# Kernel tuning notes

Hardware: AMD Instinct MI355X
Metric: run time of the kernel (lower is better)

## Reference

```python
import jax, jax.numpy as jnp
import numpy as np


def setup_inputs() -> dict:
    key = jax.random.key(0)
    k1, k2, k3, k4 = jax.random.split(key, 4)
    B, T, C, H = 8, 2048, 1024, 128
    x = jax.random.normal(k1, (B, T, C), dtype=jnp.float32)
    Wq = jax.random.normal(k2, (C, H), dtype=jnp.float32) * (C ** -0.5)
    Wk = jax.random.normal(k3, (C, H), dtype=jnp.float32) * (C ** -0.5)
    Wv = jax.random.normal(k4, (C, H), dtype=jnp.float32) * (C ** -0.5)
    return {
        "x": x, "Wq": Wq, "Wk": Wk, "Wv": Wv,
        "gamma_fast_logit": jnp.float32(0.0),
        "gamma_medium_logit": jnp.float32(2.0),
        "gamma_slow_logit": jnp.float32(4.0),
        "alpha_logits": jnp.zeros((3,), dtype=jnp.float32),
    }


def _temporal_bias(T, gamma_fast_logit, gamma_medium_logit, gamma_slow_logit, alpha_logits):
    # delta_t[i,j] = max(i-j, 0)
    i = jnp.arange(T)[:, None]
    j = jnp.arange(T)[None, :]
    delta_t = jnp.maximum(i - j, 0).astype(jnp.float32)  # (T, T)
    gf = jax.nn.sigmoid(gamma_fast_logit) * 0.3 + 0.6
    gm = jax.nn.sigmoid(gamma_medium_logit) * 0.15 + 0.85
    gs = jax.nn.sigmoid(gamma_slow_logit) * 0.05 + 0.95
    alpha = jax.nn.softmax(alpha_logits)
    mix = (alpha[0] * jnp.power(gf, delta_t)
           + alpha[1] * jnp.power(gm, delta_t)
           + alpha[2] * jnp.power(gs, delta_t))
    return jnp.log(mix + 1e-8)  # (T, T)


def reference(x, Wq, Wk, Wv, gamma_fast_logit, gamma_medium_logit, gamma_slow_logit, alpha_logits):
    B, T, C = x.shape
    H = Wq.shape[1]
    q = x @ Wq  # (B, T, H)
    k = x @ Wk
    v = x @ Wv
    scale = H ** -0.5
    wei = jnp.einsum('bth,bsh->bts', q, k) * scale  # (B, T, T)
    bias = _temporal_bias(T, gamma_fast_logit, gamma_medium_logit, gamma_slow_logit, alpha_logits)
    wei = wei + bias[None, :, :]
    causal = jnp.tril(jnp.ones((T, T), dtype=bool))
    wei = jnp.where(causal[None, :, :], wei, -jnp.inf)
    wei = jax.nn.softmax(wei, axis=-1)
    out = jnp.einsum('bts,bsh->bth', wei, v)  # (B, T, H)
    return out
```

## Files before the change

kernel.cpp:

```cpp
#include <hip/hip_runtime.h>
#include <hip/hip_bf16.h>
#include <cstdint>

typedef __attribute__((ext_vector_type(8))) short bf16x8;
typedef __attribute__((ext_vector_type(4))) float f32x4;

#define T_SEQ 2048
#define NB    8
#define CDIM  1024
#define HDIM  128
#define NQB   32

__device__ __forceinline__ float exp2fast(float x) { return __builtin_amdgcn_exp2f(x); }
__device__ __forceinline__ float log2fast(float x) { return __builtin_amdgcn_logf(x); }

__device__ __forceinline__ short f2bf(float f) {
  unsigned u = __float_as_uint(f);
  u += 0x7fff + ((u >> 16) & 1);
  return (short)(u >> 16);
}

__device__ __forceinline__ float bf2f(short s) {
  return __uint_as_float(((unsigned)(unsigned short)s) << 16);
}

__device__ __forceinline__ unsigned pk2(float a, float b) {
  return (unsigned)(unsigned short)f2bf(a) | ((unsigned)(unsigned short)f2bf(b) << 16);
}

__device__ __forceinline__ void gload_lds16(const void* gsrc, void* lds_base_uniform) {
  __builtin_amdgcn_global_load_lds(
      (const __attribute__((address_space(1))) unsigned int*)gsrc,
      (__attribute__((address_space(3))) unsigned int*)lds_base_uniform,
      16, 0, 0);
}

__global__ void msta_bias_kernel(const float* gfl, const float* gml, const float* gsl,
                                 const float* al, float* tab) {
  int d = blockIdx.x * 256 + threadIdx.x;
  if (d >= T_SEQ) return;
  float gf = 0.30f / (1.f + __expf(-gfl[0])) + 0.60f;
  float gm = 0.15f / (1.f + __expf(-gml[0])) + 0.85f;
  float gs = 0.05f / (1.f + __expf(-gsl[0])) + 0.95f;
  float a0 = al[0], a1 = al[1], a2 = al[2];
  float mx = fmaxf(a0, fmaxf(a1, a2));
  float e0 = __expf(a0 - mx), e1 = __expf(a1 - mx), e2 = __expf(a2 - mx);
  float inv = 1.f / (e0 + e1 + e2);
  float fd = (float)d;
  float mix = e0 * inv * exp2fast(fd * log2fast(gf))
            + e1 * inv * exp2fast(fd * log2fast(gm))
            + e2 * inv * exp2fast(fd * log2fast(gs));
  tab[d] = log2fast(mix + 1e-8f);
}

__global__ void msta_wt_kernel(const float* Wq, const float* Wk, const float* Wv, short* wt) {
  int idx = blockIdx.x * 256 + threadIdx.x;
  int m = idx >> 17;
  int r = idx & 131071;
  int n = r >> 10;
  int kv = r & 1023;
  const float* W = (m == 0) ? Wq : ((m == 1) ? Wk : Wv);
  float v = W[kv * HDIM + n];
  if (m == 0) v *= 0.08838834764831845f * 1.4426950408889634f;
  int c  = m * 128 + n;
  int t  = kv >> 6, kk = (kv >> 5) & 1, hi = (kv >> 3) & 3, e = kv & 7;
  int cf = c >> 4,  lo = c & 15;
  int si = (((t * 2 + kk) * 24 + cf) * 64 + (hi * 16 + lo)) * 8 + e;
  wt[si] = f2bf(v);
}

__global__ __launch_bounds__(256) void msta_qkv_kernel(
    const float* __restrict__ x, const short* __restrict__ wt,
    short* __restrict__ q, short* __restrict__ k, short* __restrict__ vt) {
  __shared__ short lds[32 * 384];

  const int tid  = threadIdx.x;
  const int lane = tid & 63;
  const int w    = tid >> 6;
  const int lo   = lane & 15, hi = lane >> 4;
  const int bid  = blockIdx.x;
  const int xcd  = bid & 7;
  const int j    = bid >> 3;
  const int r0   = (xcd * 64 + j) * 32;

  const int xrow = tid >> 3, xc8 = tid & 7;
  const float* xsrc = x + (size_t)(r0 + xrow) * CDIM + xc8 * 8;
  const int xdst = xrow * 128 + ((xc8 * 16) ^ ((xrow & 7) << 4));

  f32x4 acc[2][6];
  #pragma unroll
  for (int f = 0; f < 2; f++)
    #pragma unroll
    for (int jf = 0; jf < 6; jf++)
      acc[f][jf] = (f32x4){0.f, 0.f, 0.f, 0.f};

  float4 xa, xb;
  auto xload = [&](int t) {
    const float* s = xsrc + t * 64;
    xa = *(const float4*)s;
    xb = *(const float4*)(s + 4);
  };
  auto xwrite = [&]() {
    uint4 u;
    u.x = pk2(xa.x, xa.y); u.y = pk2(xa.z, xa.w);
    u.z = pk2(xb.x, xb.y); u.w = pk2(xb.z, xb.w);
    *(uint4*)((char*)lds + xdst) = u;
  };

  xload(0);
  for (int t = 0; t < 16; ++t) {
    xwrite();
    __syncthreads();
    if (t < 15) xload(t + 1);

    bf16x8 Bv[2][6];
    #pragma unroll
    for (int kk = 0; kk < 2; kk++)
      #pragma unroll
      for (int jf = 0; jf < 6; jf++) {
        int si = (((t * 2 + kk) * 24 + (w * 6 + jf)) * 64 + lane) * 8;
        Bv[kk][jf] = *(const bf16x8*)(wt + si);
      }

    #pragma unroll
    for (int kk = 0; kk < 2; kk++) {
      bf16x8 A[2];
      #pragma unroll
      for (int f = 0; f < 2; f++) {
        int r = f * 16 + lo;
        A[f] = *(const bf16x8*)((const char*)lds + r * 128 +
                                ((kk * 64 + hi * 16) ^ ((r & 7) << 4)));
      }
      #pragma unroll
      for (int jf = 0; jf < 6; jf++) {
        acc[0][jf] = __builtin_amdgcn_mfma_f32_16x16x32_bf16(A[0], Bv[kk][jf], acc[0][jf], 0, 0, 0);
        acc[1][jf] = __builtin_amdgcn_mfma_f32_16x16x32_bf16(A[1], Bv[kk][jf], acc[1][jf], 0, 0, 0);
      }
    }
    __syncthreads();
  }

  #pragma unroll
  for (int f = 0; f < 2; f++) {
    #pragma unroll
    for (int jf = 0; jf < 6; jf++) {
      int c = w * 96 + jf * 16 + lo;
      int row0 = f * 16 + hi * 4;
      f32x4 a = acc[f][jf];
      #pragma unroll
      for (int rg = 0; rg < 4; rg++)
        lds[(row0 + rg) * 384 + c] = f2bf(a[rg]);
    }
  }
  __syncthreads();

  #pragma unroll
  for (int p = 0; p < 2; p++) {
    int g = tid + p * 256;
    int row = g >> 4, c16 = g & 15;
    *(bf16x8*)(q + (size_t)(r0 + row) * HDIM + c16 * 8) =
        *(const bf16x8*)(lds + row * 384 + c16 * 8);
    *(bf16x8*)(k + (size_t)(r0 + row) * HDIM + c16 * 8) =
        *(const bf16x8*)(lds + row * 384 + 128 + c16 * 8);
  }
  const int bb = r0 >> 11, tt0 = r0 & 2047;
  #pragma unroll
  for (int p = 0; p < 2; p++) {
    int g = tid + p * 256;
    int h = g >> 2, rowg = g & 3;
    bf16x8 vv;
    #pragma unroll
    for (int i = 0; i < 8; i++)
      vv[i] = lds[(rowg * 8 + i) * 384 + 256 + h];
    *(bf16x8*)(vt + ((size_t)bb * HDIM + h) * T_SEQ + tt0 + rowg * 8) = vv;
  }
}

template <int SP>
__global__ __launch_bounds__(256) void msta_attn_kernel(
    const short* __restrict__ q, const short* __restrict__ kg,
    const short* __restrict__ vt, const float* __restrict__ bias_tab,
    float* __restrict__ out, short* __restrict__ opart, float2* __restrict__ ml) {
  __shared__ short Ks[64 * 128];
  __shared__ short Vs[128 * 64];
  __shared__ short Ps[4][16 * 64];

  const int tid  = threadIdx.x;
  const int lane = tid & 63;
  const int w    = tid >> 6;
  const int lo   = lane & 15, hi = lane >> 4;

  const int idx = blockIdx.x;
  const int b   = idx & 7;
  const int r_  = idx >> 3;
  const int qb  = (NQB - 1) - r_ / SP;
  const int sp  = r_ % SP;
  const int q0  = qb * 64;

  const int nt  = qb + 1;
  const int csz = (nt + SP - 1) / SP;
  const int t0  = sp * csz;
  const int t1  = (t0 + csz < nt) ? (t0 + csz) : nt;

  if (t0 >= t1) {
    if (SP > 1 && lane < 16) {
      int t = q0 + w * 16 + lane;
      ml[((size_t)sp * NB + b) * T_SEQ + t] = make_float2(-1e30f, 0.f);
    }
    return;
  }

  const short* kb = kg + (size_t)b * T_SEQ * HDIM;
  const short* vb = vt + (size_t)b * HDIM * T_SEQ;

  bf16x8 qf[4];
  const short* qbase = q + ((size_t)b * T_SEQ + q0 + w * 16 + lo) * HDIM;
  #pragma unroll
  for (int ks = 0; ks < 4; ks++)
    qf[ks] = *(const bf16x8*)(qbase + ks * 32 + hi * 8);

  const int s0i = (t1 - 1) * 64;
  const char* ksrc[4];
  const char* vsrc[4];
  #pragma unroll
  for (int i = 0; i < 4; i++) {
    int G = (w * 4 + i) * 64 + lane;
    { int r = G >> 4, g = G & 15;
      int c = (g & 8) | ((g & 7) ^ (r & 7));
      ksrc[i] = (const char*)(kb + (size_t)(s0i + r) * HDIM) + c * 16; }
    { int r = G >> 3, g = G & 7;
      int c = g ^ (r & 7);
      vsrc[i] = (const char*)(vb + (size_t)r * T_SEQ + s0i) + c * 16; }
  }
  auto stage = [&]() {
    #pragma unroll
    for (int i = 0; i < 4; i++) {
      gload_lds16(ksrc[i], (char*)Ks + (w * 4 + i) * 1024);
      ksrc[i] -= 64 * HDIM * 2;
      gload_lds16(vsrc[i], (char*)Vs + (w * 4 + i) * 1024);
      vsrc[i] -= 128;
    }
  };

  f32x4 oacc[8];
  #pragma unroll
  for (int jo = 0; jo < 8; jo++) oacc[jo] = (f32x4){0.f, 0.f, 0.f, 0.f};
  float mrow[4], lrow[4];
  #pragma unroll
  for (int rg = 0; rg < 4; rg++) { mrow[rg] = -1e30f; lrow[rg] = 0.f; }

  stage();
  __syncthreads();

  for (int t = t1 - 1; t >= t0; --t) {
    const int s0 = t * 64;

    f32x4 sacc[4];
    #pragma unroll
    for (int jf = 0; jf < 4; jf++) sacc[jf] = (f32x4){0.f, 0.f, 0.f, 0.f};
    __builtin_amdgcn_s_setprio(1);
    #pragma unroll
    for (int ks = 0; ks < 4; ks++) {
      #pragma unroll
      for (int jf = 0; jf < 4; jf++) {
        int s = jf * 16 + lo;
        int byteoff = s * 256 + ((ks * 64 + hi * 16) ^ ((s & 7) << 4));
        bf16x8 kf = *(const bf16x8*)((const char*)Ks + byteoff);
        sacc[jf] = __builtin_amdgcn_mfma_f32_16x16x32_bf16(qf[ks], kf, sacc[jf], 0, 0, 0);
      }
    }
    __builtin_amdgcn_s_setprio(0);

    float sv[4][4];
    #pragma unroll
    for (int jf = 0; jf < 4; jf++) {
      #pragma unroll
      for (int rg = 0; rg < 4; rg++) {
        int i_ = q0 + w * 16 + hi * 4 + rg;
        int j_ = s0 + jf * 16 + lo;
        int d = i_ - j_;
        sv[jf][rg] = (d >= 0) ? (sacc[jf][rg] + bias_tab[d]) : -1e30f;
      }
    }

    float mx[4];
    bool need = false;
    #pragma unroll
    for (int rg = 0; rg < 4; rg++) {
      float v = fmaxf(fmaxf(sv[0][rg], sv[1][rg]), fmaxf(sv[2][rg], sv[3][rg]));
      v = fmaxf(v, __shfl_xor(v, 1));
      v = fmaxf(v, __shfl_xor(v, 2));
      v = fmaxf(v, __shfl_xor(v, 4));
      v = fmaxf(v, __shfl_xor(v, 8));
      mx[rg] = v;
      need |= (v > mrow[rg]);
    }
    if (__any((int)need)) {
      #pragma unroll
      for (int rg = 0; rg < 4; rg++) {
        float mnew = fmaxf(mrow[rg], mx[rg]);
        float sc = exp2fast(mrow[rg] - mnew);
        mrow[rg] = mnew;
        lrow[rg] *= sc;
        #pragma unroll
        for (int jo = 0; jo < 8; jo++) oacc[jo][rg] *= sc;
      }
    }

    float psum[4] = {0.f, 0.f, 0.f, 0.f};
    #pragma unroll
    for (int jf = 0; jf < 4; jf++) {
      #pragma unroll
      for (int rg = 0; rg < 4; rg++) {
        float p = exp2fast(sv[jf][rg] - mrow[rg]);
        psum[rg] += p;
        int prow = hi * 4 + rg;
        int pcol = jf * 16 + lo;
        int byteoff = prow * 128 + ((pcol * 2) ^ ((prow & 7) << 4));
        *(short*)((char*)Ps[w] + byteoff) = f2bf(p);
      }
    }
    #pragma unroll
    for (int rg = 0; rg < 4; rg++) {
      float s = psum[rg];
      s += __shfl_xor(s, 1); s += __shfl_xor(s, 2);
      s += __shfl_xor(s, 4); s += __shfl_xor(s, 8);
      lrow[rg] += s;
    }

    __builtin_amdgcn_s_setprio(1);
    #pragma unroll
    for (int ks = 0; ks < 2; ks++) {
      int pbyte = lo * 128 + ((ks * 64 + hi * 16) ^ ((lo & 7) << 4));
      bf16x8 pf = *(const bf16x8*)((const char*)Ps[w] + pbyte);
      #pragma unroll
      for (int jo = 0; jo < 8; jo++) {
        int h = jo * 16 + lo;
        int vbyte = h * 128 + ((ks * 64 + hi * 16) ^ ((h & 7) << 4));
        bf16x8 vf = *(const bf16x8*)((const char*)Vs + vbyte);
        oacc[jo] = __builtin_amdgcn_mfma_f32_16x16x32_bf16(pf, vf, oacc[jo], 0, 0, 0);
      }
    }
    __builtin_amdgcn_s_setprio(0);

    if (t > t0) {
      __syncthreads();
      stage();
      __syncthreads();
    }
  }

  if constexpr (SP == 1) {
    #pragma unroll
    for (int jo = 0; jo < 8; jo++) {
      #pragma unroll
      for (int rg = 0; rg < 4; rg++) {
        int t = q0 + w * 16 + hi * 4 + rg;
        out[((size_t)b * T_SEQ + t) * HDIM + jo * 16 + lo] = oacc[jo][rg] / lrow[rg];
      }
    }
  } else {
    #pragma unroll
    for (int jo = 0; jo < 8; jo++) {
      #pragma unroll
      for (int rg = 0; rg < 4; rg++) {
        int t = q0 + w * 16 + hi * 4 + rg;
        opart[(((size_t)sp * NB + b) * T_SEQ + t) * HDIM + jo * 16 + lo] = f2bf(oacc[jo][rg]);
      }
    }
    if (lo == 0) {
      #pragma unroll
      for (int rg = 0; rg < 4; rg++) {
        int t = q0 + w * 16 + hi * 4 + rg;
        ml[((size_t)sp * NB + b) * T_SEQ + t] = make_float2(mrow[rg], lrow[rg]);
      }
    }
  }
}

template <int SP>
__global__ __launch_bounds__(256) void msta_merge_kernel(
    const short* __restrict__ opart, const float2* __restrict__ ml,
    float* __restrict__ out) {
  int id  = blockIdx.x * 256 + threadIdx.x;
  int row = id >> 5;
  int c4  = id & 31;

  float2 v[SP];
  float m = -1e30f;
  #pragma unroll
  for (int sp = 0; sp < SP; sp++) {
    v[sp] = ml[(size_t)sp * (NB * T_SEQ) + row];
    if (v[sp].y > 0.f) m = fmaxf(m, v[sp].x);
  }
  float denom = 0.f;
  float wgt[SP];
  #pragma unroll
  for (int sp = 0; sp < SP; sp++) {
    wgt[sp] = (v[sp].y > 0.f) ? exp2fast(v[sp].x - m) : 0.f;
    denom += wgt[sp] * v[sp].y;
  }
  float4 acc = {0.f, 0.f, 0.f, 0.f};
  #pragma unroll
  for (int sp = 0; sp < SP; sp++) {
    if (wgt[sp] != 0.f) {
      ushort4 o = *(const ushort4*)(opart + ((size_t)sp * (NB * T_SEQ) + row) * HDIM + c4 * 4);
      acc.x += wgt[sp] * bf2f((short)o.x); acc.y += wgt[sp] * bf2f((short)o.y);
      acc.z += wgt[sp] * bf2f((short)o.z); acc.w += wgt[sp] * bf2f((short)o.w);
    }
  }
  float inv = 1.f / denom;
  float4 r = make_float4(acc.x * inv, acc.y * inv, acc.z * inv, acc.w * inv);
  *(float4*)(out + (size_t)row * HDIM + c4 * 4) = r;
}

extern "C" void kernel_launch(void* const* d_in, const int* in_sizes, int n_in,
                              void* d_out, int out_size, void* d_ws, size_t ws_size,
                              hipStream_t stream) {
  (void)in_sizes; (void)n_in; (void)out_size;
  const float* x   = (const float*)d_in[0];
  const float* Wq  = (const float*)d_in[1];
  const float* Wk  = (const float*)d_in[2];
  const float* Wv  = (const float*)d_in[3];
  const float* gfl = (const float*)d_in[4];
  const float* gml = (const float*)d_in[5];
  const float* gsl = (const float*)d_in[6];
  const float* al  = (const float*)d_in[7];
  float* out = (float*)d_out;

  char* wsb = (char*)d_ws;
  float*  bias_tab = (float*)wsb;
  short*  qw   = (short*)(wsb + 8192);
  short*  kw   = (short*)(wsb + 8192 + 1 * 4194304);
  short*  vtw  = (short*)(wsb + 8192 + 2 * 4194304);
  short*  wtw  = (short*)(wsb + 8192 + 3 * 4194304);
  short*  opart = (short*)(wsb + 14680064);

  const size_t need8 = 14680064 + 8ull * 4194304 + 8ull * 131072;
  const size_t need4 = 14680064 + 4ull * 4194304 + 4ull * 131072;

  msta_bias_kernel<<<8, 256, 0, stream>>>(gfl, gml, gsl, al, bias_tab);
  msta_wt_kernel<<<1536, 256, 0, stream>>>(Wq, Wk, Wv, wtw);
  msta_qkv_kernel<<<512, 256, 0, stream>>>(x, wtw, qw, kw, vtw);

  if (ws_size >= need8) {
    float2* mlp = (float2*)(wsb + 14680064 + 8ull * 4194304);
    msta_attn_kernel<8><<<NB * NQB * 8, 256, 0, stream>>>(qw, kw, vtw, bias_tab,
                                                          nullptr, opart, mlp);
    msta_merge_kernel<8><<<(NB * T_SEQ * 32) / 256, 256, 0, stream>>>(opart, mlp, out);
  } else if (ws_size >= need4) {
    float2* mlp = (float2*)(wsb + 14680064 + 4ull * 4194304);
    msta_attn_kernel<4><<<NB * NQB * 4, 256, 0, stream>>>(qw, kw, vtw, bias_tab,
                                                          nullptr, opart, mlp);
    msta_merge_kernel<4><<<(NB * T_SEQ * 32) / 256, 256, 0, stream>>>(opart, mlp, out);
  } else {
    msta_attn_kernel<1><<<NB * NQB, 256, 0, stream>>>(qw, kw, vtw, bias_tab,
                                                      out, nullptr, nullptr);
  }
}
```

Baseline: 92.53 us.

## Split QKV projection across two column halves and add separate relayout kernel

The QKV projection kernel now launches 1024 blocks, each computing half of the 384 output columns for a 32-row tile, instead of 512 blocks computing all columns. Accumulators are written in MFMA fragment order to a scratch buffer. A new relayout kernel then gathers them into row-major q/k and transposed v. The x loads also become nontemporal. This is meant to raise parallelism and lower register and LDS pressure, but it reads x twice and adds a kernel launch plus an extra scratch round trip with scalar gathered reads.

```diff
diff --git a/kernel.cpp b/kernel.cpp
--- a/kernel.cpp
+++ b/kernel.cpp
@@ -69,10 +69,10 @@
   wt[si] = f2bf(v);
 }
 
-__global__ __launch_bounds__(256) void msta_qkv_kernel(
+__global__ __launch_bounds__(256) void msta_qkv_gemm(
     const float* __restrict__ x, const short* __restrict__ wt,
-    short* __restrict__ q, short* __restrict__ k, short* __restrict__ vt) {
-  __shared__ short lds[32 * 384];
+    short* __restrict__ scratch) {
+  __shared__ short lds[32 * 64];
 
   const int tid  = threadIdx.x;
   const int lane = tid & 63;
@@ -81,24 +81,26 @@
   const int bid  = blockIdx.x;
   const int xcd  = bid & 7;
   const int j    = bid >> 3;
-  const int r0   = (xcd * 64 + j) * 32;
+  const int cid  = j & 1;
+  const int rowblk = j >> 1;
+  const int r0   = (xcd * 64 + rowblk) * 32;
 
   const int xrow = tid >> 3, xc8 = tid & 7;
   const float* xsrc = x + (size_t)(r0 + xrow) * CDIM + xc8 * 8;
   const int xdst = xrow * 128 + ((xc8 * 16) ^ ((xrow & 7) << 4));
 
-  f32x4 acc[2][6];
+  f32x4 acc[2][3];
   #pragma unroll
   for (int f = 0; f < 2; f++)
     #pragma unroll
-    for (int jf = 0; jf < 6; jf++)
+    for (int jf = 0; jf < 3; jf++)
       acc[f][jf] = (f32x4){0.f, 0.f, 0.f, 0.f};
 
-  float4 xa, xb;
+  f32x4 xa, xb;
   auto xload = [&](int t) {
-    const float* s = xsrc + t * 64;
-    xa = *(const float4*)s;
-    xb = *(const float4*)(s + 4);
+    const f32x4* s = (const f32x4*)(xsrc + t * 64);
+    xa = __builtin_nontemporal_load(s);
+    xb = __builtin_nontemporal_load(s + 1);
   };
   auto xwrite = [&]() {
     uint4 u;
@@ -113,12 +115,12 @@
     __syncthreads();
     if (t < 15) xload(t + 1);
 
-    bf16x8 Bv[2][6];
+    bf16x8 Bv[2][3];
     #pragma unroll
     for (int kk = 0; kk < 2; kk++)
       #pragma unroll
-      for (int jf = 0; jf < 6; jf++) {
-        int si = (((t * 2 + kk) * 24 + (w * 6 + jf)) * 64 + lane) * 8;
+      for (int jf = 0; jf < 3; jf++) {
+        int si = (((t * 2 + kk) * 24 + (cid * 12 + w * 3 + jf)) * 64 + lane) * 8;
         Bv[kk][jf] = *(const bf16x8*)(wt + si);
       }
 
@@ -132,7 +134,7 @@
                                 ((kk * 64 + hi * 16) ^ ((r & 7) << 4)));
       }
       #pragma unroll
-      for (int jf = 0; jf < 6; jf++) {
+      for (int jf = 0; jf < 3; jf++) {
         acc[0][jf] = __builtin_amdgcn_mfma_f32_16x16x32_bf16(A[0], Bv[kk][jf], acc[0][jf], 0, 0, 0);
         acc[1][jf] = __builtin_amdgcn_mfma_f32_16x16x32_bf16(A[1], Bv[kk][jf], acc[1][jf], 0, 0, 0);
       }
@@ -140,39 +142,66 @@
     __syncthreads();
   }
 
+  short* sb = scratch + (size_t)bid * 6144;
   #pragma unroll
   for (int f = 0; f < 2; f++) {
     #pragma unroll
-    for (int jf = 0; jf < 6; jf++) {
-      int c = w * 96 + jf * 16 + lo;
-      int row0 = f * 16 + hi * 4;
+    for (int jf = 0; jf < 3; jf++) {
       f32x4 a = acc[f][jf];
-      #pragma unroll
-      for (int rg = 0; rg < 4; rg++)
-        lds[(row0 + rg) * 384 + c] = f2bf(a[rg]);
-    }
-  }
-  __syncthreads();
-
-  #pragma unroll
-  for (int p = 0; p < 2; p++) {
-    int g = tid + p * 256;
-    int row = g >> 4, c16 = g & 15;
-    *(bf16x8*)(q + (size_t)(r0 + row) * HDIM + c16 * 8) =
-        *(const bf16x8*)(lds + row * 384 + c16 * 8);
-    *(bf16x8*)(k + (size_t)(r0 + row) * HDIM + c16 * 8) =
-        *(const bf16x8*)(lds + row * 384 + 128 + c16 * 8);
-  }
-  const int bb = r0 >> 11, tt0 = r0 & 2047;
-  #pragma unroll
-  for (int p = 0; p < 2; p++) {
-    int g = tid + p * 256;
-    int h = g >> 2, rowg = g & 3;
-    bf16x8 vv;
+      uint2 pr;
+      pr.x = pk2(a[0], a[1]);
+      pr.y = pk2(a[2], a[3]);
+      *(uint2*)(sb + (f * 3 + jf) * 1024 + tid * 4) = pr;
+    }
+  }
+}
+
+__device__ __forceinline__ short read_scr(const short* scratch, int rb, int row, int c) {
+  int xcd = rb >> 6, rowblk = rb & 63;
+  int cid = c / 192;
+  int cl  = c - cid * 192;
+  int w_  = cl / 48;
+  int jf  = (cl % 48) >> 4;
+  int lo_ = cl & 15;
+  int f_  = row >> 4;
+  int hi_ = (row >> 2) & 3;
+  int rg  = row & 3;
+  int bid = (((rowblk << 1) + cid) << 3) + xcd;
+  return scratch[(((size_t)bid * 6 + f_ * 3 + jf) << 10) + ((w_ * 64 + hi_ * 16 + lo_) << 2) + rg];
+}
+
+__global__ __launch_bounds__(256) void msta_relayout(
+    const short* __restrict__ scratch,
+    short* __restrict__ q, short* __restrict__ k, short* __restrict__ vt) {
+  const int tid = threadIdx.x;
+  if (blockIdx.x < 2048) {
+    int g   = blockIdx.x * 256 + tid;
+    int rb  = g >> 10;
+    int rem = g & 1023;
+    int row = rem >> 5;
+    int cg  = rem & 31;
+    int r0  = rb * 32;
+    bf16x8 v;
     #pragma unroll
     for (int i = 0; i < 8; i++)
-      vv[i] = lds[(rowg * 8 + i) * 384 + 256 + h];
-    *(bf16x8*)(vt + ((size_t)bb * HDIM + h) * T_SEQ + tt0 + rowg * 8) = vv;
+      v[i] = read_scr(scratch, rb, row, cg * 8 + i);
+    if (cg < 16)
+      *(bf16x8*)(q + (size_t)(r0 + row) * HDIM + cg * 8) = v;
+    else
+      *(bf16x8*)(k + (size_t)(r0 + row) * HDIM + (cg - 16) * 8) = v;
+  } else {
+    int g   = (blockIdx.x - 2048) * 256 + tid;
+    int rb  = g >> 9;
+    int rem = g & 511;
+    int h   = rem >> 2;
+    int rowg = rem & 3;
+    int r0  = rb * 32;
+    int bb  = r0 >> 11, tt0 = r0 & 2047;
+    bf16x8 v;
+    #pragma unroll
+    for (int i = 0; i < 8; i++)
+      v[i] = read_scr(scratch, rb, rowg * 8 + i, 256 + h);
+    *(bf16x8*)(vt + ((size_t)bb * HDIM + h) * T_SEQ + tt0 + rowg * 8) = v;
   }
 }
 
@@ -434,14 +463,18 @@
   short*  kw   = (short*)(wsb + 8192 + 1 * 4194304);
   short*  vtw  = (short*)(wsb + 8192 + 2 * 4194304);
   short*  wtw  = (short*)(wsb + 8192 + 3 * 4194304);
-  short*  opart = (short*)(wsb + 14680064);
+  short*  scratch = (short*)(wsb + 14680064);
+  short*  opart   = (short*)(wsb + 14680064);
 
   const size_t need8 = 14680064 + 8ull * 4194304 + 8ull * 131072;
   const size_t need4 = 14680064 + 4ull * 4194304 + 4ull * 131072;
+  const size_t need1 = 14680064 + 12582912;
 
   msta_bias_kernel<<<8, 256, 0, stream>>>(gfl, gml, gsl, al, bias_tab);
   msta_wt_kernel<<<1536, 256, 0, stream>>>(Wq, Wk, Wv, wtw);
-  msta_qkv_kernel<<<512, 256, 0, stream>>>(x, wtw, qw, kw, vtw);
+  msta_qkv_gemm<<<1024, 256, 0, stream>>>(x, wtw, scratch);
+  msta_relayout<<<3072, 256, 0, stream>>>(scratch, qw, kw, vtw);
+  (void)need1;
 
   if (ws_size >= need8) {
     float2* mlp = (float2*)(wsb + 14680064 + 8ull * 4194304);
```

Result: slower. 111.8 us (+20.8%).

## Double-buffer x tile in QKV projection with 64-row, 512-thread blocks

Applied to the files above, without the earlier changes.

The QKV projection kernel now processes 64 rows per block with 8 waves instead of 32 rows with 4 waves. Each wave computes 48 output columns across 4 row fragments, which halves the per-wave weight-fragment loads relative to the MFMA count. The x tile is double-buffered in LDS so the next tile's global load and LDS write overlap compute, removing one barrier per iteration, and x loads become nontemporal. The launch drops to 256 blocks, which lowers grid parallelism and raises per-block LDS use.

```diff
diff --git a/kernel.cpp b/kernel.cpp
--- a/kernel.cpp
+++ b/kernel.cpp
@@ -69,10 +69,10 @@
   wt[si] = f2bf(v);
 }
 
-__global__ __launch_bounds__(256) void msta_qkv_kernel(
+__global__ __launch_bounds__(512) void msta_qkv_kernel(
     const float* __restrict__ x, const short* __restrict__ wt,
     short* __restrict__ q, short* __restrict__ k, short* __restrict__ vt) {
-  __shared__ short lds[32 * 384];
+  __shared__ short lds[64 * 384];
 
   const int tid  = threadIdx.x;
   const int lane = tid & 63;
@@ -80,73 +80,73 @@
   const int lo   = lane & 15, hi = lane >> 4;
   const int bid  = blockIdx.x;
   const int xcd  = bid & 7;
-  const int j    = bid >> 3;
-  const int r0   = (xcd * 64 + j) * 32;
+  const int rowblk = bid >> 3;
+  const int r0   = xcd * 2048 + rowblk * 64;
 
   const int xrow = tid >> 3, xc8 = tid & 7;
   const float* xsrc = x + (size_t)(r0 + xrow) * CDIM + xc8 * 8;
   const int xdst = xrow * 128 + ((xc8 * 16) ^ ((xrow & 7) << 4));
 
-  f32x4 acc[2][6];
-  #pragma unroll
-  for (int f = 0; f < 2; f++)
-    #pragma unroll
-    for (int jf = 0; jf < 6; jf++)
-      acc[f][jf] = (f32x4){0.f, 0.f, 0.f, 0.f};
-
-  float4 xa, xb;
+  f32x4 acc[4][3];
+  #pragma unroll
+  for (int rf = 0; rf < 4; rf++)
+    #pragma unroll
+    for (int jf = 0; jf < 3; jf++)
+      acc[rf][jf] = (f32x4){0.f, 0.f, 0.f, 0.f};
+
+  f32x4 xa, xb;
   auto xload = [&](int t) {
-    const float* s = xsrc + t * 64;
-    xa = *(const float4*)s;
-    xb = *(const float4*)(s + 4);
+    const f32x4* s = (const f32x4*)(xsrc + t * 64);
+    xa = __builtin_nontemporal_load(s);
+    xb = __builtin_nontemporal_load(s + 1);
   };
-  auto xwrite = [&]() {
+  auto xwrite = [&](int buf) {
     uint4 u;
     u.x = pk2(xa.x, xa.y); u.y = pk2(xa.z, xa.w);
     u.z = pk2(xb.x, xb.y); u.w = pk2(xb.z, xb.w);
-    *(uint4*)((char*)lds + xdst) = u;
+    *(uint4*)((char*)lds + buf * 8192 + xdst) = u;
   };
 
   xload(0);
+  xwrite(0);
+  __syncthreads();
+
   for (int t = 0; t < 16; ++t) {
-    xwrite();
+    const int buf = t & 1;
+    if (t < 15) xload(t + 1);
+
+    bf16x8 Bv[2][3];
+    #pragma unroll
+    for (int kk = 0; kk < 2; kk++)
+      #pragma unroll
+      for (int jf = 0; jf < 3; jf++) {
+        int si = (((t * 2 + kk) * 24 + (w * 3 + jf)) * 64 + lane) * 8;
+        Bv[kk][jf] = *(const bf16x8*)(wt + si);
+      }
+
+    #pragma unroll
+    for (int kk = 0; kk < 2; kk++) {
+      #pragma unroll
+      for (int rf = 0; rf < 4; rf++) {
+        int r = rf * 16 + lo;
+        bf16x8 A = *(const bf16x8*)((const char*)lds + buf * 8192 + r * 128 +
+                                    ((kk * 64 + hi * 16) ^ ((r & 7) << 4)));
+        #pragma unroll
+        for (int jf = 0; jf < 3; jf++)
+          acc[rf][jf] = __builtin_amdgcn_mfma_f32_16x16x32_bf16(A, Bv[kk][jf], acc[rf][jf], 0, 0, 0);
+      }
+    }
+    if (t < 15) xwrite(buf ^ 1);
     __syncthreads();
-    if (t < 15) xload(t + 1);
-
-    bf16x8 Bv[2][6];
-    #pragma unroll
-    for (int kk = 0; kk < 2; kk++)
-      #pragma unroll
-      for (int jf = 0; jf < 6; jf++) {
-        int si = (((t * 2 + kk) * 24 + (w * 6 + jf)) * 64 + lane) * 8;
-        Bv[kk][jf] = *(const bf16x8*)(wt + si);
-      }
-
-    #pragma unroll
-    for (int kk = 0; kk < 2; kk++) {
-      bf16x8 A[2];
-      #pragma unroll
-      for (int f = 0; f < 2; f++) {
-        int r = f * 16 + lo;
-        A[f] = *(const bf16x8*)((const char*)lds + r * 128 +
-                                ((kk * 64 + hi * 16) ^ ((r & 7) << 4)));
-      }
-      #pragma unroll
-      for (int jf = 0; jf < 6; jf++) {
-        acc[0][jf] = __builtin_amdgcn_mfma_f32_16x16x32_bf16(A[0], Bv[kk][jf], acc[0][jf], 0, 0, 0);
-        acc[1][jf] = __builtin_amdgcn_mfma_f32_16x16x32_bf16(A[1], Bv[kk][jf], acc[1][jf], 0, 0, 0);
-      }
-    }
-    __syncthreads();
-  }
-
-  #pragma unroll
-  for (int f = 0; f < 2; f++) {
-    #pragma unroll
-    for (int jf = 0; jf < 6; jf++) {
-      int c = w * 96 + jf * 16 + lo;
-      int row0 = f * 16 + hi * 4;
-      f32x4 a = acc[f][jf];
+  }
+
+  #pragma unroll
+  for (int rf = 0; rf < 4; rf++) {
+    #pragma unroll
+    for (int jf = 0; jf < 3; jf++) {
+      int c = w * 48 + jf * 16 + lo;
+      int row0 = rf * 16 + hi * 4;
+      f32x4 a = acc[rf][jf];
       #pragma unroll
       for (int rg = 0; rg < 4; rg++)
         lds[(row0 + rg) * 384 + c] = f2bf(a[rg]);
@@ -156,7 +156,7 @@
 
   #pragma unroll
   for (int p = 0; p < 2; p++) {
-    int g = tid + p * 256;
+    int g = tid + p * 512;
     int row = g >> 4, c16 = g & 15;
     *(bf16x8*)(q + (size_t)(r0 + row) * HDIM + c16 * 8) =
         *(const bf16x8*)(lds + row * 384 + c16 * 8);
@@ -166,8 +166,8 @@
   const int bb = r0 >> 11, tt0 = r0 & 2047;
   #pragma unroll
   for (int p = 0; p < 2; p++) {
-    int g = tid + p * 256;
-    int h = g >> 2, rowg = g & 3;
+    int g = tid + p * 512;
+    int h = g >> 3, rowg = g & 7;
     bf16x8 vv;
     #pragma unroll
     for (int i = 0; i < 8; i++)
@@ -441,7 +441,7 @@
 
   msta_bias_kernel<<<8, 256, 0, stream>>>(gfl, gml, gsl, al, bias_tab);
   msta_wt_kernel<<<1536, 256, 0, stream>>>(Wq, Wk, Wv, wtw);
-  msta_qkv_kernel<<<512, 256, 0, stream>>>(x, wtw, qw, kw, vtw);
+  msta_qkv_kernel<<<256, 512, 0, stream>>>(x, wtw, qw, kw, vtw);
 
   if (ws_size >= need8) {
     float2* mlp = (float2*)(wsb + 14680064 + 8ull * 4194304);
```

Measured after the change: 91.15 us. No clear change (-1.5%).
